# Performance work log

Measured on AMD Instinct MI355X. Metric: run time of the kernel, lower is better.

## Reference

```python
import jax, jax.numpy as jnp
import numpy as np

DIM_IN, DIM_Q, DIM_K = 768, 64, 64
B, S = 8, 2048

def setup_inputs() -> dict:
    key = jax.random.key(0)
    ks = jax.random.split(key, 9)
    lim_q = 1.0 / np.sqrt(DIM_IN)
    return {
        'query': jax.random.normal(ks[0], (B, S, DIM_IN), jnp.float32),
        'key':   jax.random.normal(ks[1], (B, S, DIM_IN), jnp.float32),
        'value': jax.random.normal(ks[2], (B, S, DIM_IN), jnp.float32),
        'Wq': jax.random.uniform(ks[3], (DIM_IN, DIM_Q), jnp.float32, -lim_q, lim_q),
        'bq': jax.random.uniform(ks[4], (DIM_Q,), jnp.float32, -lim_q, lim_q),
        'Wk': jax.random.uniform(ks[5], (DIM_IN, DIM_K), jnp.float32, -lim_q, lim_q),
        'bk': jax.random.uniform(ks[6], (DIM_K,), jnp.float32, -lim_q, lim_q),
        'Wv': jax.random.uniform(ks[7], (DIM_IN, DIM_K), jnp.float32, -lim_q, lim_q),
        'bv': jax.random.uniform(ks[8], (DIM_K,), jnp.float32, -lim_q, lim_q),
    }

def reference(query, key, value, Wq, bq, Wk, bk, Wv, bv):
    # linear projections: [B,S,dim_in] -> [B,S,64]
    q = jnp.einsum('bsd,dq->bsq', query, Wq) + bq
    k = jnp.einsum('bsd,dk->bsk', key, Wk) + bk
    v = jnp.einsum('bsd,dk->bsk', value, Wv) + bv
    # cosine attention: L2-normalize q and k along feature dim
    qn = q / jnp.linalg.norm(q, axis=-1, keepdims=True)
    kn = k / jnp.linalg.norm(k, axis=-1, keepdims=True)
    scale = jnp.sqrt(jnp.asarray(q.shape[-1], q.dtype))  # scaled=True
    scores = jnp.einsum('bqk,bsk->bqs', qn, kn) / scale  # [B,S,S]
    attn = jax.nn.softmax(scores, axis=-1)
    return jnp.einsum('bqs,bsk->bqk', attn, v)  # [B,S,64]
```

## Files before the change

### kernel.cpp

```cpp
#include <hip/hip_runtime.h>
#include <hip/hip_bf16.h>

#define DIN 768
#define DD  64
#define NB  8
#define SS  2048
#define NROWS (NB*SS)

typedef __bf16 bf16;
typedef __attribute__((ext_vector_type(8))) __bf16 bf16x8;
typedef __attribute__((ext_vector_type(4))) __bf16 bf16x4;
typedef __attribute__((ext_vector_type(4))) float f32x4;

#define MFMA16 __builtin_amdgcn_mfma_f32_16x16x32_bf16


__global__ __launch_bounds__(256) void k_wt(const float* __restrict__ Wq,
                                            const float* __restrict__ Wk,
                                            const float* __restrict__ Wv,
                                            bf16* __restrict__ wt)
{
    int t = blockIdx.y;
    const float* W = (t == 0) ? Wq : ((t == 1) ? Wk : Wv);
    bf16* o = wt + (size_t)t * DD * DIN;
    int k0 = blockIdx.x * 64;

    __shared__ float tile[64][65];

    #pragma unroll
    for (int i = 0; i < 4; ++i) {
        int idx = threadIdx.x + i * 256;
        int row = idx >> 4;
        int c4  = (idx & 15) * 4;
        f32x4 u = *(const f32x4*)(W + (size_t)(k0 + row) * DD + c4);
        tile[c4 + 0][row] = u[0]; tile[c4 + 1][row] = u[1];
        tile[c4 + 2][row] = u[2]; tile[c4 + 3][row] = u[3];
    }
    __syncthreads();
    #pragma unroll
    for (int i = 0; i < 4; ++i) {
        int idx = threadIdx.x + i * 256;
        int col = idx >> 4;
        int k4  = (idx & 15) * 4;
        bf16x4 u;
        u[0] = (bf16)tile[col][k4 + 0]; u[1] = (bf16)tile[col][k4 + 1];
        u[2] = (bf16)tile[col][k4 + 2]; u[3] = (bf16)tile[col][k4 + 3];
        *(bf16x4*)(o + (size_t)col * DIN + k0 + k4) = u;
    }
}

__global__ __launch_bounds__(256) void k_proj(
    const float* __restrict__ Xq, const float* __restrict__ Xk, const float* __restrict__ Xv,
    const float* __restrict__ bq, const float* __restrict__ bk, const float* __restrict__ bv,
    const bf16* __restrict__ wt,
    bf16* __restrict__ qn, bf16* __restrict__ kn, bf16* __restrict__ vT)
{
    int t = blockIdx.y;
    const float* X    = (t == 0) ? Xq : ((t == 1) ? Xk : Xv);
    const float* bias = (t == 0) ? bq : ((t == 1) ? bk : bv);
    const bf16*  w    = wt + (size_t)t * DD * DIN;

    int row0 = blockIdx.x * 64;
    int lane = threadIdx.x & 63;
    int wid  = threadIdx.x >> 6;
    int lr = lane & 15, lk = lane >> 4;
    int r  = row0 + wid * 16 + lr;

    const float* xp = X + (size_t)r * DIN + lk * 8;
    const bf16*  wp = w + (size_t)lr * DIN + lk * 8;

    f32x4 acc[4] = {};

    #pragma unroll 4
    for (int kk = 0; kk < DIN; kk += 32) {
        f32x4 x0 = *(const f32x4*)(xp + kk);
        f32x4 x1 = *(const f32x4*)(xp + kk + 4);
        bf16x8 a;
        a[0] = (bf16)x0[0]; a[1] = (bf16)x0[1]; a[2] = (bf16)x0[2]; a[3] = (bf16)x0[3];
        a[4] = (bf16)x1[0]; a[5] = (bf16)x1[1]; a[6] = (bf16)x1[2]; a[7] = (bf16)x1[3];
        #pragma unroll
        for (int cf = 0; cf < 4; ++cf) {
            bf16x8 bfr = *(const bf16x8*)(wp + (size_t)cf * 16 * DIN + kk);
            acc[cf] = MFMA16(a, bfr, acc[cf], 0, 0, 0);
        }
    }

    #pragma unroll
    for (int cf = 0; cf < 4; ++cf) {
        float bc = bias[cf * 16 + lr];
        acc[cf][0] += bc; acc[cf][1] += bc; acc[cf][2] += bc; acc[cf][3] += bc;
    }

    if (t < 2) {
        const float c = (t == 0) ? 0.18033688011112042f  : 1.0f;
        f32x4 ss = {};
        #pragma unroll
        for (int cf = 0; cf < 4; ++cf)
            #pragma unroll
            for (int reg = 0; reg < 4; ++reg)
                ss[reg] += acc[cf][reg] * acc[cf][reg];
        #pragma unroll
        for (int reg = 0; reg < 4; ++reg) {
            float v = ss[reg];
            v += __shfl_xor(v, 1); v += __shfl_xor(v, 2);
            v += __shfl_xor(v, 4); v += __shfl_xor(v, 8);
            ss[reg] = v;
        }
        bf16* o = (t == 0) ? qn : kn;
        #pragma unroll
        for (int reg = 0; reg < 4; ++reg) {
            float sc = __builtin_amdgcn_rsqf(ss[reg]) * c;
            int rr = row0 + wid * 16 + lk * 4 + reg;
            #pragma unroll
            for (int cf = 0; cf < 4; ++cf)
                o[(size_t)rr * DD + cf * 16 + lr] = (bf16)(acc[cf][reg] * sc);
        }
    } else {
        __shared__ bf16 vt[64][72];
        #pragma unroll
        for (int reg = 0; reg < 4; ++reg)
            #pragma unroll
            for (int cf = 0; cf < 4; ++cf)
                vt[cf * 16 + lr][wid * 16 + lk * 4 + reg] = (bf16)acc[cf][reg];
        __syncthreads();
        int bb = row0 >> 11, s0 = row0 & (SS - 1);
        #pragma unroll
        for (int j = 0; j < 4; ++j) {
            int f4 = threadIdx.x + j * 256;
            int dv = f4 >> 4, s4 = f4 & 15;
            bf16x4 u;
            u[0] = vt[dv][s4 * 4 + 0]; u[1] = vt[dv][s4 * 4 + 1];
            u[2] = vt[dv][s4 * 4 + 2]; u[3] = vt[dv][s4 * 4 + 3];
            *(bf16x4*)(vT + ((size_t)(bb * DD + dv)) * SS + s0 + s4 * 4) = u;
        }
    }
}

__global__ __launch_bounds__(256) void k_attn(
    const bf16* __restrict__ qn, const bf16* __restrict__ kn,
    const bf16* __restrict__ vT, float* __restrict__ out)
{
    int b  = blockIdx.y;
    int q0 = blockIdx.x * 32;
    int lane = threadIdx.x & 63, wid = threadIdx.x >> 6;
    int lr = lane & 15, lk = lane >> 4;

    __shared__ bf16  p_all[4][32 * 64];
    __shared__ float num_lds[4][32][68];
    __shared__ float den_lds[4][32];
    bf16* p_lds = &p_all[wid][0];

    const bf16* qb = qn + ((size_t)(b * SS + q0 + lr)) * DD + lk * 8;
    bf16x8 qf[2][2];
    qf[0][0] = *(const bf16x8*)(qb);
    qf[0][1] = *(const bf16x8*)(qb + 32);
    qf[1][0] = *(const bf16x8*)(qb + 16 * DD);
    qf[1][1] = *(const bf16x8*)(qb + 16 * DD + 32);

    const bf16* kb = kn + (size_t)b * SS * DD;
    const bf16* vb = vT + (size_t)b * DD * SS;

    f32x4 oacc[2][4] = {};
    f32x4 den[2]     = {};

    int sbeg = wid * (SS / 4);
    for (int s = sbeg; s < sbeg + SS / 4; s += 64) {
        f32x4 sacc[2][4] = {};
        #pragma unroll
        for (int cf = 0; cf < 4; ++cf) {
            const bf16* kp = kb + (size_t)(s + cf * 16 + lr) * DD + lk * 8;
            bf16x8 k0 = *(const bf16x8*)(kp);
            bf16x8 k1 = *(const bf16x8*)(kp + 32);
            sacc[0][cf] = MFMA16(qf[0][0], k0, sacc[0][cf], 0, 0, 0);
            sacc[0][cf] = MFMA16(qf[0][1], k1, sacc[0][cf], 0, 0, 0);
            sacc[1][cf] = MFMA16(qf[1][0], k0, sacc[1][cf], 0, 0, 0);
            sacc[1][cf] = MFMA16(qf[1][1], k1, sacc[1][cf], 0, 0, 0);
        }
        #pragma unroll
        for (int rf = 0; rf < 2; ++rf)
            #pragma unroll
            for (int reg = 0; reg < 4; ++reg) {
                int prow = rf * 16 + lk * 4 + reg;
                int swz  = (prow & 7) << 4;
                #pragma unroll
                for (int cf = 0; cf < 4; ++cf) {
                    float p = __builtin_amdgcn_exp2f(sacc[rf][cf][reg]);
                    den[rf][reg] += p;
                    *(bf16*)((char*)p_lds + prow * 128 + ((((cf * 16 + lr) * 2)) ^ swz)) = (bf16)p;
                }
            }
        __builtin_amdgcn_sched_barrier(0);
        bf16x8 pf[2][2];
        #pragma unroll
        for (int rf = 0; rf < 2; ++rf)
            #pragma unroll
            for (int ks = 0; ks < 2; ++ks) {
                int prow = rf * 16 + lr;
                int swz  = (prow & 7) << 4;
                pf[rf][ks] = *(const bf16x8*)((char*)p_lds + prow * 128
                               + (((ks * 32 + lk * 8) * 2) ^ swz));
            }
        #pragma unroll
        for (int cf = 0; cf < 4; ++cf) {
            const bf16* vp = vb + (size_t)(cf * 16 + lr) * SS + s + lk * 8;
            bf16x8 v0 = *(const bf16x8*)(vp);
            bf16x8 v1 = *(const bf16x8*)(vp + 32);
            oacc[0][cf] = MFMA16(pf[0][0], v0, oacc[0][cf], 0, 0, 0);
            oacc[0][cf] = MFMA16(pf[0][1], v1, oacc[0][cf], 0, 0, 0);
            oacc[1][cf] = MFMA16(pf[1][0], v0, oacc[1][cf], 0, 0, 0);
            oacc[1][cf] = MFMA16(pf[1][1], v1, oacc[1][cf], 0, 0, 0);
        }
    }

    #pragma unroll
    for (int rf = 0; rf < 2; ++rf)
        #pragma unroll
        for (int reg = 0; reg < 4; ++reg) {
            float d = den[rf][reg];
            d += __shfl_xor(d, 1); d += __shfl_xor(d, 2);
            d += __shfl_xor(d, 4); d += __shfl_xor(d, 8);
            if (lr == 0) den_lds[wid][rf * 16 + lk * 4 + reg] = d;
            #pragma unroll
            for (int cf = 0; cf < 4; ++cf)
                num_lds[wid][rf * 16 + lk * 4 + reg][cf * 16 + lr] = oacc[rf][cf][reg];
        }
    __syncthreads();

    float* ob = out + ((size_t)b * SS + q0) * DD;
    #pragma unroll
    for (int j = 0; j < 8; ++j) {
        int e = threadIdx.x + j * 256;
        int q = e >> 6, dv = e & 63;
        float n = num_lds[0][q][dv] + num_lds[1][q][dv] + num_lds[2][q][dv] + num_lds[3][q][dv];
        float d = den_lds[0][q] + den_lds[1][q] + den_lds[2][q] + den_lds[3][q];
        ob[e] = n / d;
    }
}

extern "C" void kernel_launch(void* const* d_in, const int* in_sizes, int n_in,
                              void* d_out, int out_size, void* d_ws, size_t ws_size,
                              hipStream_t stream) {
    const float* Xq = (const float*)d_in[0];
    const float* Xk = (const float*)d_in[1];
    const float* Xv = (const float*)d_in[2];
    const float* Wq = (const float*)d_in[3];
    const float* bq = (const float*)d_in[4];
    const float* Wk = (const float*)d_in[5];
    const float* bk = (const float*)d_in[6];
    const float* Wv = (const float*)d_in[7];
    const float* bv = (const float*)d_in[8];

    bf16* ws = (bf16*)d_ws;
    bf16* wt = ws;
    bf16* qn = ws + 3 * DD * DIN;
    bf16* kn = qn + (size_t)NROWS * DD;
    bf16* vT = kn + (size_t)NROWS * DD;
    float* o = (float*)d_out;

    hipLaunchKernelGGL(k_wt,   dim3(12, 3),  dim3(256), 0, stream, Wq, Wk, Wv, wt);
    hipLaunchKernelGGL(k_proj, dim3(256, 3), dim3(256), 0, stream,
                       Xq, Xk, Xv, bq, bk, bv, wt, qn, kn, vT);
    hipLaunchKernelGGL(k_attn, dim3(64, 8),  dim3(256), 0, stream, qn, kn, vT, o);
}
```

Before: 229.1 us.

## Prefetch projection operands in registers and halve attention query tile

The projection kernel's K loop is fully unrolled with a three-stage register prefetch of X and W fragments, to hide global load latency behind MFMAs. The attention kernel now processes 16 query rows per block instead of 32, doubling the grid to raise occupancy and shrink per-wave register and LDS use. The P scratch buffer now aliases the numerator LDS area. Each K/V tile is reused by half as many queries, so global/L2 traffic for K and V doubles.

```diff
diff --git a/kernel.cpp b/kernel.cpp
--- a/kernel.cpp
+++ b/kernel.cpp
@@ -71,18 +71,39 @@
 
     f32x4 acc[4] = {};
 
-    #pragma unroll 4
-    for (int kk = 0; kk < DIN; kk += 32) {
-        f32x4 x0 = *(const f32x4*)(xp + kk);
-        f32x4 x1 = *(const f32x4*)(xp + kk + 4);
+    f32x4  px0[3], px1[3];
+    bf16x8 pw[3][4];
+    #pragma unroll
+    for (int p = 0; p < 3; ++p) {
+        int kk = p * 32;
+        px0[p] = *(const f32x4*)(xp + kk);
+        px1[p] = *(const f32x4*)(xp + kk + 4);
+        #pragma unroll
+        for (int cf = 0; cf < 4; ++cf)
+            pw[p][cf] = *(const bf16x8*)(wp + (size_t)cf * 16 * DIN + kk);
+    }
+
+    #pragma unroll
+    for (int it = 0; it < 24; ++it) {
+        const int slot = it % 3;
         bf16x8 a;
-        a[0] = (bf16)x0[0]; a[1] = (bf16)x0[1]; a[2] = (bf16)x0[2]; a[3] = (bf16)x0[3];
-        a[4] = (bf16)x1[0]; a[5] = (bf16)x1[1]; a[6] = (bf16)x1[2]; a[7] = (bf16)x1[3];
-        #pragma unroll
-        for (int cf = 0; cf < 4; ++cf) {
-            bf16x8 bfr = *(const bf16x8*)(wp + (size_t)cf * 16 * DIN + kk);
-            acc[cf] = MFMA16(a, bfr, acc[cf], 0, 0, 0);
-        }
+        a[0] = (bf16)px0[slot][0]; a[1] = (bf16)px0[slot][1];
+        a[2] = (bf16)px0[slot][2]; a[3] = (bf16)px0[slot][3];
+        a[4] = (bf16)px1[slot][0]; a[5] = (bf16)px1[slot][1];
+        a[6] = (bf16)px1[slot][2]; a[7] = (bf16)px1[slot][3];
+        bf16x8 w0 = pw[slot][0], w1 = pw[slot][1], w2 = pw[slot][2], w3 = pw[slot][3];
+        if (it + 3 < 24) {
+            int kk = (it + 3) * 32;
+            px0[slot] = *(const f32x4*)(xp + kk);
+            px1[slot] = *(const f32x4*)(xp + kk + 4);
+            #pragma unroll
+            for (int cf = 0; cf < 4; ++cf)
+                pw[slot][cf] = *(const bf16x8*)(wp + (size_t)cf * 16 * DIN + kk);
+        }
+        acc[0] = MFMA16(a, w0, acc[0], 0, 0, 0);
+        acc[1] = MFMA16(a, w1, acc[1], 0, 0, 0);
+        acc[2] = MFMA16(a, w2, acc[2], 0, 0, 0);
+        acc[3] = MFMA16(a, w3, acc[3], 0, 0, 0);
     }
 
     #pragma unroll
@@ -141,97 +162,82 @@
     const bf16* __restrict__ vT, float* __restrict__ out)
 {
     int b  = blockIdx.y;
-    int q0 = blockIdx.x * 32;
+    int q0 = blockIdx.x * 16;
     int lane = threadIdx.x & 63, wid = threadIdx.x >> 6;
     int lr = lane & 15, lk = lane >> 4;
 
-    __shared__ bf16  p_all[4][32 * 64];
-    __shared__ float num_lds[4][32][68];
-    __shared__ float den_lds[4][32];
-    bf16* p_lds = &p_all[wid][0];
+    __shared__ float num_all[4][16][68];
+    __shared__ float den_lds[4][16];
+    bf16* p_lds = (bf16*)&num_all[wid][0][0];
+    float (*num_lds)[68] = num_all[wid];
 
     const bf16* qb = qn + ((size_t)(b * SS + q0 + lr)) * DD + lk * 8;
-    bf16x8 qf[2][2];
-    qf[0][0] = *(const bf16x8*)(qb);
-    qf[0][1] = *(const bf16x8*)(qb + 32);
-    qf[1][0] = *(const bf16x8*)(qb + 16 * DD);
-    qf[1][1] = *(const bf16x8*)(qb + 16 * DD + 32);
+    bf16x8 qf0 = *(const bf16x8*)(qb);
+    bf16x8 qf1 = *(const bf16x8*)(qb + 32);
 
     const bf16* kb = kn + (size_t)b * SS * DD;
     const bf16* vb = vT + (size_t)b * DD * SS;
 
-    f32x4 oacc[2][4] = {};
-    f32x4 den[2]     = {};
+    f32x4 oacc[4] = {};
+    f32x4 den     = {};
 
     int sbeg = wid * (SS / 4);
     for (int s = sbeg; s < sbeg + SS / 4; s += 64) {
-        f32x4 sacc[2][4] = {};
+        f32x4 sacc[4] = {};
         #pragma unroll
         for (int cf = 0; cf < 4; ++cf) {
             const bf16* kp = kb + (size_t)(s + cf * 16 + lr) * DD + lk * 8;
             bf16x8 k0 = *(const bf16x8*)(kp);
             bf16x8 k1 = *(const bf16x8*)(kp + 32);
-            sacc[0][cf] = MFMA16(qf[0][0], k0, sacc[0][cf], 0, 0, 0);
-            sacc[0][cf] = MFMA16(qf[0][1], k1, sacc[0][cf], 0, 0, 0);
-            sacc[1][cf] = MFMA16(qf[1][0], k0, sacc[1][cf], 0, 0, 0);
-            sacc[1][cf] = MFMA16(qf[1][1], k1, sacc[1][cf], 0, 0, 0);
-        }
-        #pragma unroll
-        for (int rf = 0; rf < 2; ++rf)
-            #pragma unroll
-            for (int reg = 0; reg < 4; ++reg) {
-                int prow = rf * 16 + lk * 4 + reg;
-                int swz  = (prow & 7) << 4;
-                #pragma unroll
-                for (int cf = 0; cf < 4; ++cf) {
-                    float p = __builtin_amdgcn_exp2f(sacc[rf][cf][reg]);
-                    den[rf][reg] += p;
-                    *(bf16*)((char*)p_lds + prow * 128 + ((((cf * 16 + lr) * 2)) ^ swz)) = (bf16)p;
-                }
+            sacc[cf] = MFMA16(qf0, k0, sacc[cf], 0, 0, 0);
+            sacc[cf] = MFMA16(qf1, k1, sacc[cf], 0, 0, 0);
+        }
+        #pragma unroll
+        for (int reg = 0; reg < 4; ++reg) {
+            int prow = lk * 4 + reg;
+            int swz  = (prow & 7) << 4;
+            #pragma unroll
+            for (int cf = 0; cf < 4; ++cf) {
+                float p = __builtin_amdgcn_exp2f(sacc[cf][reg]);
+                den[reg] += p;
+                *(bf16*)((char*)p_lds + prow * 128 + ((((cf * 16 + lr) * 2)) ^ swz)) = (bf16)p;
             }
+        }
         __builtin_amdgcn_sched_barrier(0);
-        bf16x8 pf[2][2];
-        #pragma unroll
-        for (int rf = 0; rf < 2; ++rf)
-            #pragma unroll
-            for (int ks = 0; ks < 2; ++ks) {
-                int prow = rf * 16 + lr;
-                int swz  = (prow & 7) << 4;
-                pf[rf][ks] = *(const bf16x8*)((char*)p_lds + prow * 128
-                               + (((ks * 32 + lk * 8) * 2) ^ swz));
-            }
+        bf16x8 pf0, pf1;
+        {
+            int swz = (lr & 7) << 4;
+            pf0 = *(const bf16x8*)((char*)p_lds + lr * 128 + (((lk * 8) * 2) ^ swz));
+            pf1 = *(const bf16x8*)((char*)p_lds + lr * 128 + (((32 + lk * 8) * 2) ^ swz));
+        }
         #pragma unroll
         for (int cf = 0; cf < 4; ++cf) {
             const bf16* vp = vb + (size_t)(cf * 16 + lr) * SS + s + lk * 8;
             bf16x8 v0 = *(const bf16x8*)(vp);
             bf16x8 v1 = *(const bf16x8*)(vp + 32);
-            oacc[0][cf] = MFMA16(pf[0][0], v0, oacc[0][cf], 0, 0, 0);
-            oacc[0][cf] = MFMA16(pf[0][1], v1, oacc[0][cf], 0, 0, 0);
-            oacc[1][cf] = MFMA16(pf[1][0], v0, oacc[1][cf], 0, 0, 0);
-            oacc[1][cf] = MFMA16(pf[1][1], v1, oacc[1][cf], 0, 0, 0);
-        }
-    }
-
-    #pragma unroll
-    for (int rf = 0; rf < 2; ++rf)
-        #pragma unroll
-        for (int reg = 0; reg < 4; ++reg) {
-            float d = den[rf][reg];
-            d += __shfl_xor(d, 1); d += __shfl_xor(d, 2);
-            d += __shfl_xor(d, 4); d += __shfl_xor(d, 8);
-            if (lr == 0) den_lds[wid][rf * 16 + lk * 4 + reg] = d;
-            #pragma unroll
-            for (int cf = 0; cf < 4; ++cf)
-                num_lds[wid][rf * 16 + lk * 4 + reg][cf * 16 + lr] = oacc[rf][cf][reg];
-        }
+            oacc[cf] = MFMA16(pf0, v0, oacc[cf], 0, 0, 0);
+            oacc[cf] = MFMA16(pf1, v1, oacc[cf], 0, 0, 0);
+        }
+    }
+
+    #pragma unroll
+    for (int reg = 0; reg < 4; ++reg) {
+        float d = den[reg];
+        d += __shfl_xor(d, 1); d += __shfl_xor(d, 2);
+        d += __shfl_xor(d, 4); d += __shfl_xor(d, 8);
+        if (lr == 0) den_lds[wid][lk * 4 + reg] = d;
+        #pragma unroll
+        for (int cf = 0; cf < 4; ++cf)
+            num_lds[lk * 4 + reg][cf * 16 + lr] = oacc[cf][reg];
+    }
     __syncthreads();
 
     float* ob = out + ((size_t)b * SS + q0) * DD;
     #pragma unroll
-    for (int j = 0; j < 8; ++j) {
+    for (int j = 0; j < 4; ++j) {
         int e = threadIdx.x + j * 256;
         int q = e >> 6, dv = e & 63;
-        float n = num_lds[0][q][dv] + num_lds[1][q][dv] + num_lds[2][q][dv] + num_lds[3][q][dv];
+        float n = num_all[0][q][dv] + num_all[1][q][dv] + num_all[2][q][dv] + num_all[3][q][dv];
         float d = den_lds[0][q] + den_lds[1][q] + den_lds[2][q] + den_lds[3][q];
         ob[e] = n / d;
     }
@@ -260,5 +266,5 @@
     hipLaunchKernelGGL(k_wt,   dim3(12, 3),  dim3(256), 0, stream, Wq, Wk, Wv, wt);
     hipLaunchKernelGGL(k_proj, dim3(256, 3), dim3(256), 0, stream,
                        Xq, Xk, Xv, bq, bk, bv, wt, qn, kn, vT);
-    hipLaunchKernelGGL(k_attn, dim3(64, 8),  dim3(256), 0, stream, qn, kn, vT, o);
-}
+    hipLaunchKernelGGL(k_attn, dim3(128, 8), dim3(256), 0, stream, qn, kn, vT, o);
+}
```

After: 250.5 us. 9.3% more time.
